# Optimization experiments

Measured on AMD Instinct MI355X. Metric: run time of the kernel, lower is better.

Reference implementation:

```python
import jax, jax.numpy as jnp
import numpy as np

B, N_PER, DEG, F_IN, F_HID = 64, 1024, 16, 128, 128
E = B * N_PER * DEG  # 1,048,576 edges, grouped per graph


def setup_inputs() -> dict:
    key = jax.random.key(0)
    ks = jax.random.split(key, 16)
    n_total = B * N_PER
    x = jax.random.normal(ks[0], (n_total, F_IN), dtype=jnp.float32)
    # edges are random within each graph block
    local = jax.random.randint(ks[1], (2, E), 0, N_PER)
    offs = (jnp.arange(E, dtype=jnp.int64) // (N_PER * DEG)) * N_PER
    edge_index = (local.astype(jnp.int64) + offs[None, :])
    edge_weight = jax.random.uniform(ks[2], (E,), dtype=jnp.float32)
    batch_index = jnp.repeat(jnp.arange(B, dtype=jnp.int64), N_PER)
    s = 1.0 / np.sqrt(F_HID)
    params = {
        'W1': jax.random.normal(ks[3], (F_IN, F_HID)) * s,
        'b1': jnp.zeros((F_HID,), jnp.float32),
        'p1': jax.random.normal(ks[4], (F_HID,)) * s,
        'W2': jax.random.normal(ks[5], (F_HID, F_HID)) * s,
        'b2': jnp.zeros((F_HID,), jnp.float32),
        'p2': jax.random.normal(ks[6], (F_HID,)) * s,
        'W3': jax.random.normal(ks[7], (F_HID, F_HID)) * s,
        'b3': jnp.zeros((F_HID,), jnp.float32),
        'p3': jax.random.normal(ks[8], (F_HID,)) * s,
        'Wo': jax.random.normal(ks[9], (2 * F_HID, 1)) * s,
        'bo': jnp.zeros((1,), jnp.float32),
    }
    return {'x': x, 'edge_index': edge_index, 'edge_weight': edge_weight,
            'batch_index': batch_index, **params}


def _gcn_conv(x, src, dst, w, W, b):
    # GCNConv with add_self_loops=True, symmetric normalization, edge_weight.
    n = x.shape[0]
    xW = x @ W
    deg = jnp.zeros((n,), x.dtype).at[dst].add(w) + 1.0  # +1 from self-loop fill
    dinv = jax.lax.rsqrt(deg)
    norm = dinv[src] * w * dinv[dst]
    agg = jnp.zeros_like(xW).at[dst].add(norm[:, None] * xW[src])
    return agg + (dinv * dinv)[:, None] * xW + b  # self-loop term + bias


def _topk_pool(x, src, dst, w, p, n, k):
    # TopKPooling with nonlinearity=sigmoid, equal-size graphs (n -> k nodes).
    f = x.shape[1]
    xr = x.reshape(B, n, f)
    score = jax.nn.sigmoid((xr @ p) / jnp.linalg.norm(p))  # [B, n]
    vals, perm = jax.lax.top_k(score, k)                    # per-graph top-k
    xn = jnp.take_along_axis(xr, perm[:, :, None], axis=1) * vals[:, :, None]
    # inverse map old local idx -> new local idx (-1 if dropped)
    inv = jnp.full((B, n), -1, dtype=jnp.int32)
    inv = inv.at[jnp.arange(B)[:, None], perm].set(jnp.arange(k, dtype=jnp.int32)[None, :])
    g = src // n
    sl = inv[g, src % n]
    dl = inv[dst // n, dst % n]
    keep = (sl >= 0) & (dl >= 0)
    # dropped edges are masked to node 0 with weight 0 (contribute nothing)
    src2 = jnp.where(keep, g * k + sl, 0)
    dst2 = jnp.where(keep, (dst // n) * k + dl, 0)
    w2 = jnp.where(keep, w, jnp.zeros((), w.dtype))
    return xn.reshape(B * k, f), src2, dst2, w2


def reference(x, edge_index, edge_weight, batch_index,
              W1, b1, p1, W2, b2, p2, W3, b3, p3, Wo, bo):
    src, dst = edge_index[0], edge_index[1]
    w = edge_weight
    n = N_PER
    h = _gcn_conv(x, src, dst, w, W1, b1)
    h, src, dst, w = _topk_pool(h, src, dst, w, p1, n, n // 2); n //= 2
    h = jax.nn.relu(h)
    h = _gcn_conv(h, src, dst, w, W2, b2)
    h, src, dst, w = _topk_pool(h, src, dst, w, p2, n, n // 2); n //= 2
    h = jax.nn.relu(h)
    h = _gcn_conv(h, src, dst, w, W3, b3)
    h, src, dst, w = _topk_pool(h, src, dst, w, p3, n, n // 2); n //= 2
    h = jax.nn.relu(h)
    hr = h.reshape(B, n, -1)
    cat = jnp.concatenate([hr.max(axis=1), hr.mean(axis=1)], axis=1)  # gmp || gap
    out = jax.nn.sigmoid(cat @ Wo + bo)
    return out, cat
```

## Files before the change

kernel.cpp:

```cpp
#include <hip/hip_runtime.h>

#define NB 64
#define EDGES 1048576
#define NTOT  65536

struct __align__(8) CsrE { int s; float w; };

using bf16x8 = __attribute__((ext_vector_type(8))) short;
using f32x4  = __attribute__((ext_vector_type(4))) float;

__global__ void k_zerof(float* __restrict__ p, int n){
  int i=blockIdx.x*256+threadIdx.x; if(i<n) p[i]=0.f;
}

__device__ inline void split1(float x, unsigned &hi16, unsigned &lo16){
  unsigned b=__float_as_uint(x);
  unsigned h=(b+0x7FFFu+((b>>16)&1u))&0xFFFF0000u;
  float lf=x-__uint_as_float(h);
  unsigned lb=__float_as_uint(lf);
  hi16=h>>16;
  lo16=(lb+0x7FFFu+((lb>>16)&1u))>>16;
}

__device__ inline void split8(const float4&u, const float4&v, bf16x8&hi, bf16x8&lo){
  float e[8]={u.x,u.y,u.z,u.w,v.x,v.y,v.z,v.w};
  #pragma unroll
  for(int j=0;j<8;++j){
    unsigned h16,l16; split1(e[j],h16,l16);
    hi[j]=(short)h16; lo[j]=(short)l16;
  }
}

template<bool G, int S>
__global__ __launch_bounds__(256) void mm_mfma(const float* __restrict__ X,
        const float* __restrict__ W, const int* __restrict__ selold,
        const float* __restrict__ score, float* __restrict__ Y, int gshift){
  __shared__ __align__(16) unsigned Wl[16384];
  const int RPB = 64*S;
  int b=blockIdx.x;
  int xcd=b&7, slot=b>>3, bpg=1<<gshift;
  int graph=xcd*8+(slot>>gshift), idx=slot&(bpg-1);
  int row0b = graph*(bpg*RPB) + idx*RPB;
  for(int t=threadIdx.x;t<8192;t+=256){
    int i=t&3, l=(t>>2)&63, c=(t>>8)&7, q=(t>>11)&3;
    int col=c*16+(l&15);
    int k0=q*32+((l>>4)<<3)+i*2;
    float x0=W[k0*128+col], x1=W[(k0+1)*128+col];
    unsigned h0,l0,h1,l1;
    split1(x0,h0,l0); split1(x1,h1,l1);
    int base=((q*8+c)*2)*256;
    Wl[base + l*4 + i]       = (h1<<16)|h0;
    Wl[base + 256 + l*4 + i] = (l1<<16)|l0;
  }
  const int wave=threadIdx.x>>6, lane=threadIdx.x&63;
  const int row0 = row0b + wave*(16*S);
  const int lrow=lane&15, lko=(lane>>4)<<3;
  int orow[S]; float scr[S];
  #pragma unroll
  for(int s=0;s<S;++s){
    int rr=row0+s*16+lrow;
    orow[s]=G?selold[rr]:rr;
    scr[s]=G?score[orow[s]]:1.f;
  }
  const f32x4 vzero={0.f,0.f,0.f,0.f};
  f32x4 acc[S][8];
  #pragma unroll
  for(int s=0;s<S;++s){
    #pragma unroll
    for(int c=0;c<8;++c) acc[s][c]=vzero;
  }
  __syncthreads();
  const char* wb=(const char*)Wl + lane*16;
  float4 u[S],v[S];
  #pragma unroll
  for(int s=0;s<S;++s){
    const float* xp=X+(size_t)orow[s]*128+lko;
    u[s]=*(const float4*)xp; v[s]=*(const float4*)(xp+4);
  }
  #pragma unroll
  for(int q=0;q<4;++q){
    float4 un[S],vn[S];
    if(q<3){
      #pragma unroll
      for(int s=0;s<S;++s){
        const float* xp=X+(size_t)orow[s]*128+(q+1)*32+lko;
        un[s]=*(const float4*)xp; vn[s]=*(const float4*)(xp+4);
      }
    }
    bf16x8 Ah[S],Al[S];
    #pragma unroll
    for(int s=0;s<S;++s){
      if(G){
        u[s].x=fmaxf(u[s].x*scr[s],0.f); u[s].y=fmaxf(u[s].y*scr[s],0.f);
        u[s].z=fmaxf(u[s].z*scr[s],0.f); u[s].w=fmaxf(u[s].w*scr[s],0.f);
        v[s].x=fmaxf(v[s].x*scr[s],0.f); v[s].y=fmaxf(v[s].y*scr[s],0.f);
        v[s].z=fmaxf(v[s].z*scr[s],0.f); v[s].w=fmaxf(v[s].w*scr[s],0.f);
      }
      split8(u[s],v[s],Ah[s],Al[s]);
    }
    #pragma unroll
    for(int c=0;c<8;++c){
      const bf16x8 bh=*(const bf16x8*)(wb + (q*8+c)*2048);
      const bf16x8 bl=*(const bf16x8*)(wb + (q*8+c)*2048 + 1024);
      #pragma unroll
      for(int s=0;s<S;++s){
        acc[s][c]=__builtin_amdgcn_mfma_f32_16x16x32_bf16(Ah[s],bh,acc[s][c],0,0,0);
        acc[s][c]=__builtin_amdgcn_mfma_f32_16x16x32_bf16(Al[s],bh,acc[s][c],0,0,0);
        acc[s][c]=__builtin_amdgcn_mfma_f32_16x16x32_bf16(Ah[s],bl,acc[s][c],0,0,0);
      }
    }
    if(q<3){
      #pragma unroll
      for(int s=0;s<S;++s){ u[s]=un[s]; v[s]=vn[s]; }
    }
  }
  const int dcol=lane&15, dr0=(lane>>4)<<2;
  #pragma unroll
  for(int s=0;s<S;++s){
    #pragma unroll
    for(int c=0;c<8;++c){
      #pragma unroll
      for(int r=0;r<4;++r){
        Y[(size_t)(row0+s*16+dr0+r)*128 + c*16 + dcol]=acc[s][c][r];
      }
    }
  }
}

__global__ __launch_bounds__(1024) void k_csr(const int* __restrict__ esrc,
        const int* __restrict__ edst, const float* __restrict__ ew,
        int* __restrict__ rowptr, float* __restrict__ dinv1, CsrE* __restrict__ csr){
  __shared__ int lc[1024];
  __shared__ float lw[1024];
  __shared__ int wsum[16];
  int g=blockIdx.x, i=threadIdx.x;
  int lane=i&63, w=i>>6;
  int e0=g*16384;
  lc[i]=0; lw[i]=0.f;
  __syncthreads();
  for(int e=e0+i; e<e0+16384; e+=1024){
    int dl=edst[e]&1023;
    atomicAdd(&lc[dl],1);
    atomicAdd(&lw[dl],ew[e]);
  }
  __syncthreads();
  int c=lc[i]; float wsv=lw[i];
  int v=c;
  #pragma unroll
  for(int off=1;off<64;off<<=1){ int t=__shfl_up(v,off,64); if(lane>=off) v+=t; }
  if(lane==63) wsum[w]=v;
  __syncthreads();
  int base=0;
  for(int k=0;k<w;++k) base+=wsum[k];
  int excl=base+v-c;
  rowptr[g*1024+i]=e0+excl;
  dinv1[g*1024+i]=rsqrtf(wsv+1.0f);
  if(g==63 && i==1023) rowptr[65536]=EDGES;
  __syncthreads();
  lc[i]=e0+excl;
  __syncthreads();
  for(int e=e0+i; e<e0+16384; e+=1024){
    int dl=edst[e]&1023;
    int pos=atomicAdd(&lc[dl],1);
    CsrE ce; ce.s=esrc[e]; ce.w=ew[e];
    csr[pos]=ce;
  }
}

template<bool F>
__global__ __launch_bounds__(256) void k_gather(const float* __restrict__ xw, const CsrE* __restrict__ csr,
        const int* __restrict__ rowptr, const int* __restrict__ map, const int* __restrict__ inv,
        const float* __restrict__ dinvv, const float* __restrict__ bias, const float* __restrict__ p,
        float* __restrict__ h, float* __restrict__ score, int gshift, int ns){
  int wv=threadIdx.x>>6, half=(threadIdx.x>>5)&1, hl=threadIdx.x&31;
  int b=blockIdx.x, xcd=b&7, slot=b>>3, bpg=1<<gshift;
  int graph=xcd*8+(slot>>gshift), idx=slot&(bpg-1);
  int v = graph*(bpg<<3) + (idx<<3) + wv*2 + half;
  if(v>=ns) return;
  int d0 = F? map[v] : v;
  float dv=dinvv[v];
  int rs=rowptr[d0], re=rowptr[d0+1];
  const int f4=hl*4;
  float4 accA={0.f,0.f,0.f,0.f}, accB={0.f,0.f,0.f,0.f};
  for(int base=rs; base<re; base+=32){
    int len=re-base; if(len>32) len=32;
    int sidx=0; float cf=0.f;
    if(hl<len){
      CsrE en=csr[base+hl];
      int s=en.s; bool live=true;
      if(F){ int t=inv[s]; live=(t>=0); s=live?t:0; }
      if(live){ sidx=s; cf=dinvv[s]*en.w; }
    }
    int len8=(len+7)&~7;
    for(int j=0;j<len8;j+=8){
      float cc[8]; int ss[8];
      #pragma unroll
      for(int m=0;m<8;++m){ cc[m]=__shfl(cf,j+m,32); ss[m]=__shfl(sidx,j+m,32); }
      float4 xv_[8];
      #pragma unroll
      for(int m=0;m<8;++m) xv_[m]=*(const float4*)&xw[(size_t)ss[m]*128+f4];
      #pragma unroll
      for(int m=0;m<8;m+=2){
        accA.x+=cc[m]*xv_[m].x; accA.y+=cc[m]*xv_[m].y;
        accA.z+=cc[m]*xv_[m].z; accA.w+=cc[m]*xv_[m].w;
        accB.x+=cc[m+1]*xv_[m+1].x; accB.y+=cc[m+1]*xv_[m+1].y;
        accB.z+=cc[m+1]*xv_[m+1].z; accB.w+=cc[m+1]*xv_[m+1].w;
      }
    }
  }
  float4 acc; acc.x=accA.x+accB.x; acc.y=accA.y+accB.y;
  acc.z=accA.z+accB.z; acc.w=accA.w+accB.w;
  const float4 xv=*(const float4*)&xw[(size_t)v*128+f4];
  const float4 bv=*(const float4*)&bias[f4];
  float d2=dv*dv;
  float4 hv;
  hv.x=acc.x*dv + d2*xv.x + bv.x;
  hv.y=acc.y*dv + d2*xv.y + bv.y;
  hv.z=acc.z*dv + d2*xv.z + bv.z;
  hv.w=acc.w*dv + d2*xv.w + bv.w;
  *(float4*)&h[(size_t)v*128+f4]=hv;
  const float4 pv=*(const float4*)&p[f4];
  float z=hv.x*pv.x+hv.y*pv.y+hv.z*pv.z+hv.w*pv.w;
  float pp=pv.x*pv.x+pv.y*pv.y+pv.z*pv.z+pv.w*pv.w;
  #pragma unroll
  for(int m=16;m>0;m>>=1){ z+=__shfl_xor(z,m,32); pp+=__shfl_xor(pp,m,32); }
  if(hl==0) score[v]=1.0f/(1.0f+expf(-z/sqrtf(pp)));
}

template<int N, int K, int MODE>
__global__ __launch_bounds__(N) void k_topk(const float* __restrict__ score,
        int* __restrict__ inv, int* __restrict__ selold,
        const int* __restrict__ inv1s, const int* __restrict__ sel1s,
        int* __restrict__ inv12, int* __restrict__ map12,
        const int* __restrict__ rowptr, const CsrE* __restrict__ csr,
        float* __restrict__ dinv_out,
        const float* __restrict__ h3, const float* __restrict__ Wo,
        const float* __restrict__ bo, float* __restrict__ outp){
  __shared__ unsigned hist[256];
  __shared__ int wsum[16];
  __shared__ int c_sh, r_sh;
  __shared__ float red2[256];
  __shared__ int sOld[128];
  __shared__ float sSc[128];
  int g=blockIdx.x, i=threadIdx.x;
  int lane=i&63, w=i>>6;
  int gv=g*N+i;
  unsigned key=__float_as_uint(score[gv]);
  int st=1;
  int R=K;
  #pragma unroll
  for(int pass=0; pass<4; ++pass){
    int shift=24-pass*8;
    if(i<256) hist[i]=0;
    __syncthreads();
    unsigned byte=(key>>shift)&255u;
    if(st==1) atomicAdd(&hist[byte],1u);
    __syncthreads();
    unsigned hcnt=0, sfx=0;
    if(i<256){
      hcnt=hist[i]; sfx=hcnt;
      #pragma unroll
      for(int off=1;off<64;off<<=1){
        unsigned t=__shfl_down(sfx,off,64);
        if(lane+off<64) sfx+=t;
      }
      if(lane==0) wsum[w]=(int)sfx;
    }
    __syncthreads();
    if(i<256){
      int tot=0;
      for(int k=w+1;k<4;++k) tot+=wsum[k];
      int Si=(int)sfx+tot;
      int A=Si-(int)hcnt;
      if(A<R && R<=Si){ c_sh=i; r_sh=R-A; }
    }
    __syncthreads();
    int c=c_sh; R=r_sh;
    if(st==1){
      if((int)byte>c) st=2;
      else if((int)byte<c) st=0;
    }
    __syncthreads();
  }
  int alive=(st==1)?1:0;
  unsigned long long mA=__ballot(alive);
  int rA=__popcll(mA & ((1ULL<<lane)-1ULL));
  if(lane==0) wsum[w]=__popcll(mA);
  __syncthreads();
  int offA=0;
  for(int k=0;k<w;++k) offA+=wsum[k];
  int tie_rank=offA+rA;
  int sel=(st==2)||(st==1 && tie_rank<R);
  __syncthreads();
  unsigned long long mS=__ballot(sel);
  int rS=__popcll(mS & ((1ULL<<lane)-1ULL));
  if(lane==0) wsum[w]=__popcll(mS);
  __syncthreads();
  int offS=0;
  for(int k=0;k<w;++k) offS+=wsum[k];
  int ng=g*K+offS+rS;
  if(sel && ng<NB*K){ inv[gv]=ng; selold[ng]=gv; }
  else inv[gv]=-1;
  if(MODE==1){
    __syncthreads();
    for(int t=i; t<K; t+=N){
      int v=g*K+t;
      int d0=selold[v];
      int rs=rowptr[d0], re=rowptr[d0+1];
      float s0=0.f,s1=0.f,s2=0.f,s3=0.f;
      int e=rs;
      for(; e+4<=re; e+=4){
        CsrE e0=csr[e], e1=csr[e+1], e2=csr[e+2], e3=csr[e+3];
        if(inv[e0.s]>=0) s0+=e0.w;
        if(inv[e1.s]>=0) s1+=e1.w;
        if(inv[e2.s]>=0) s2+=e2.w;
        if(inv[e3.s]>=0) s3+=e3.w;
      }
      for(; e<re; ++e){
        CsrE en=csr[e];
        if(inv[en.s]>=0) s0+=en.w;
      }
      dinv_out[v]=rsqrtf((s0+s1)+(s2+s3)+1.0f);
    }
  }
  if(MODE==2){
    __syncthreads();
    for(int t=i; t<1024; t+=N){
      int v0=g*1024+t;
      int q=inv1s[v0];
      inv12[v0]=(q>=0)?inv[q]:-1;
    }
    for(int t=i; t<K; t+=N){
      int v=g*K+t;
      map12[v]=sel1s[selold[v]];
    }
    __syncthreads();
    for(int t=i; t<K; t+=N){
      int v=g*K+t;
      int d0=map12[v];
      int rs=rowptr[d0], re=rowptr[d0+1];
      float s0=0.f,s1=0.f,s2=0.f,s3=0.f;
      int e=rs;
      for(; e+4<=re; e+=4){
        CsrE e0=csr[e], e1=csr[e+1], e2=csr[e+2], e3=csr[e+3];
        if(inv12[e0.s]>=0) s0+=e0.w;
        if(inv12[e1.s]>=0) s1+=e1.w;
        if(inv12[e2.s]>=0) s2+=e2.w;
        if(inv12[e3.s]>=0) s3+=e3.w;
      }
      for(; e<re; ++e){
        CsrE en=csr[e];
        if(inv12[en.s]>=0) s0+=en.w;
      }
      dinv_out[v]=rsqrtf((s0+s1)+(s2+s3)+1.0f);
    }
  }
  if(MODE==3){
    __syncthreads();
    if(i<128){ int o=selold[g*128+i]; sOld[i]=o; sSc[i]=score[o]; }
    __syncthreads();
    int f=i&127, hf=i>>7;
    float mx=-3.4e38f, sm=0.f;
    #pragma unroll 4
    for(int nd=hf*64; nd<hf*64+64; ++nd){
      float vv=fmaxf(h3[(size_t)sOld[nd]*128+f]*sSc[nd],0.f);
      mx=fmaxf(mx,vv); sm+=vv;
    }
    red2[i]=mx; __syncthreads();
    float mx2 = (hf==0)? fmaxf(mx,red2[i+128]) : 0.f;
    __syncthreads();
    red2[i]=sm; __syncthreads();
    if(hf==0){
      float smT=sm+red2[i+128];
      float mean=smT*(1.0f/128.0f);
      outp[64+g*256+f]    =mx2;
      outp[64+g*256+128+f]=mean;
    }
    __syncthreads();
    if(hf==0) red2[f]=mx2*Wo[f]+( (sm+red2[f+128]) * (1.0f/128.0f))*Wo[128+f];
    __syncthreads();
    for(int off=64;off>0;off>>=1){
      if(i<off) red2[i]+=red2[i+off];
      __syncthreads();
    }
    if(i==0){ float z=red2[0]+bo[0]; outp[g]=1.0f/(1.0f+expf(-z)); }
  }
}

extern "C" void kernel_launch(void* const* d_in, const int* in_sizes, int n_in,
                              void* d_out, int out_size, void* d_ws, size_t ws_size,
                              hipStream_t stream) {
  (void)in_sizes; (void)n_in;
  const float* x  = (const float*)d_in[0];
  const int*   ei = (const int*)d_in[1];
  const float* ew = (const float*)d_in[2];
  const float* W1=(const float*)d_in[4];  const float* b1=(const float*)d_in[5];  const float* p1=(const float*)d_in[6];
  const float* W2=(const float*)d_in[7];  const float* b2=(const float*)d_in[8];  const float* p2=(const float*)d_in[9];
  const float* W3=(const float*)d_in[10]; const float* b3=(const float*)d_in[11]; const float* p3=(const float*)d_in[12];
  const float* Wo=(const float*)d_in[13]; const float* bo=(const float*)d_in[14];
  float* out=(float*)d_out;

  char* ws=(char*)d_ws;
  size_t cur=0;
  float* slot0=(float*)(ws+cur); cur+=33554432;
  float* slot1=(float*)(ws+cur); cur+=33554432;
  CsrE*  csr  =(CsrE*)(ws+cur);  cur+=(size_t)EDGES*8;
  int*   rowptr=(int*) (ws+cur); cur+=262400;
  float* dinv1=(float*)(ws+cur); cur+=262144;
  float* dinv2=(float*)(ws+cur); cur+=131072;
  float* dinv3=(float*)(ws+cur); cur+=65536;
  float* sc1  =(float*)(ws+cur); cur+=262144;
  float* sc2  =(float*)(ws+cur); cur+=131072;
  float* sc3  =(float*)(ws+cur); cur+=65536;
  int*   inv1 =(int*)  (ws+cur); cur+=262144;
  int*   inv2 =(int*)  (ws+cur); cur+=131072;
  int*   invS =(int*)  (ws+cur); cur+=65536;
  int*   inv12=(int*)  (ws+cur); cur+=262144;
  int*   sel1 =(int*)  (ws+cur); cur+=131072;
  int*   sel2 =(int*)  (ws+cur); cur+=65536;
  int*   sel3 =(int*)  (ws+cur); cur+=32768;
  int*   map12=(int*)  (ws+cur); cur+=65536;

  if (ws_size < cur) {
    k_zerof<<<(out_size+255)/256,256,0,stream>>>(out,out_size);
    return;
  }

  const int* esrc=ei; const int* edst=ei+EDGES;

  mm_mfma<false,2><<<NTOT/128,256,0,stream>>>(x,W1,nullptr,nullptr,slot0,3);
  k_csr<<<NB,1024,0,stream>>>(esrc,edst,ew,rowptr,dinv1,csr);
  k_gather<false><<<NTOT/8,256,0,stream>>>(slot0,csr,rowptr,nullptr,nullptr,
                                           dinv1,b1,p1,slot1,sc1,7,NTOT);
  k_topk<1024,512,1><<<NB,1024,0,stream>>>(sc1,inv1,sel1,nullptr,nullptr,nullptr,nullptr,
                                           rowptr,csr,dinv2,nullptr,nullptr,nullptr,nullptr);

  mm_mfma<true,1><<<32768/64,256,0,stream>>>(slot1,W2,sel1,sc1,slot0,3);
  k_gather<true><<<32768/8,256,0,stream>>>(slot0,csr,rowptr,sel1,inv1,
                                           dinv2,b2,p2,slot1,sc2,6,32768);
  k_topk<512,256,2><<<NB,512,0,stream>>>(sc2,inv2,sel2,inv1,sel1,inv12,map12,
                                         rowptr,csr,dinv3,nullptr,nullptr,nullptr,nullptr);

  mm_mfma<true,1><<<16384/64,256,0,stream>>>(slot1,W3,sel2,sc2,slot0,2);
  k_gather<true><<<16384/8,256,0,stream>>>(slot0,csr,rowptr,map12,inv12,
                                           dinv3,b3,p3,slot1,sc3,5,16384);
  k_topk<256,128,3><<<NB,256,0,stream>>>(sc3,invS,sel3,nullptr,nullptr,nullptr,nullptr,
                                         nullptr,nullptr,nullptr,slot1,Wo,bo,out);
}
```

Baseline: 311.6 us.

## Split CSR build into chunked count, scan, and global-atomic scatter kernels

The single 64-block CSR construction kernel becomes three kernels: a 256-block per-chunk degree count, a per-graph scan that sums the four chunk counts, and a 256-block scatter that uses global atomics on fill pointers. The goal is to spread the edge-processing work over four times as many blocks, since 64 blocks leave most of the GPU's compute units idle. In exchange it adds two kernel launches, extra global traffic for the chunk arrays, and slower global atomics in place of LDS atomics during the scatter.

Result: no change. 309.5 us (-0.7%).

```diff
diff --git a/kernel.cpp b/kernel.cpp
--- a/kernel.cpp
+++ b/kernel.cpp
@@ -127,24 +127,35 @@
   }
 }
 
-__global__ __launch_bounds__(1024) void k_csr(const int* __restrict__ esrc,
-        const int* __restrict__ edst, const float* __restrict__ ew,
-        int* __restrict__ rowptr, float* __restrict__ dinv1, CsrE* __restrict__ csr){
+__global__ __launch_bounds__(1024) void k_count(const int* __restrict__ edst,
+        const float* __restrict__ ew, int* __restrict__ chunkcnt, float* __restrict__ chunkw){
   __shared__ int lc[1024];
   __shared__ float lw[1024];
+  int b=blockIdx.x, i=threadIdx.x;
+  int xcd=b&7, slot=b>>3;
+  int graph=xcd*8+(slot&7), chunk=slot>>3;
+  int e0=graph*16384+chunk*4096;
+  lc[i]=0; lw[i]=0.f;
+  __syncthreads();
+  for(int e=e0+i; e<e0+4096; e+=1024){
+    int dl=edst[e]&1023;
+    atomicAdd(&lc[dl],1);
+    atomicAdd(&lw[dl],ew[e]);
+  }
+  __syncthreads();
+  chunkcnt[chunk*65536+graph*1024+i]=lc[i];
+  chunkw  [chunk*65536+graph*1024+i]=lw[i];
+}
+
+__global__ __launch_bounds__(1024) void k_scan_graph(const int* __restrict__ chunkcnt,
+        const float* __restrict__ chunkw, int* __restrict__ rowptr,
+        float* __restrict__ dinv1, int* __restrict__ fill){
   __shared__ int wsum[16];
   int g=blockIdx.x, i=threadIdx.x;
   int lane=i&63, w=i>>6;
-  int e0=g*16384;
-  lc[i]=0; lw[i]=0.f;
-  __syncthreads();
-  for(int e=e0+i; e<e0+16384; e+=1024){
-    int dl=edst[e]&1023;
-    atomicAdd(&lc[dl],1);
-    atomicAdd(&lw[dl],ew[e]);
-  }
-  __syncthreads();
-  int c=lc[i]; float wsv=lw[i];
+  int o=g*1024+i;
+  int c = chunkcnt[o]+chunkcnt[65536+o]+chunkcnt[131072+o]+chunkcnt[196608+o];
+  float ws = chunkw[o]+chunkw[65536+o]+chunkw[131072+o]+chunkw[196608+o];
   int v=c;
   #pragma unroll
   for(int off=1;off<64;off<<=1){ int t=__shfl_up(v,off,64); if(lane>=off) v+=t; }
@@ -153,15 +164,24 @@
   int base=0;
   for(int k=0;k<w;++k) base+=wsum[k];
   int excl=base+v-c;
-  rowptr[g*1024+i]=e0+excl;
-  dinv1[g*1024+i]=rsqrtf(wsv+1.0f);
+  int e0=g*16384;
+  rowptr[o]=e0+excl;
+  fill[o]=e0+excl;
+  dinv1[o]=rsqrtf(ws+1.0f);
   if(g==63 && i==1023) rowptr[65536]=EDGES;
-  __syncthreads();
-  lc[i]=e0+excl;
-  __syncthreads();
-  for(int e=e0+i; e<e0+16384; e+=1024){
+}
+
+__global__ __launch_bounds__(1024) void k_scatter2(const int* __restrict__ esrc,
+        const int* __restrict__ edst, const float* __restrict__ ew,
+        int* __restrict__ fill, CsrE* __restrict__ csr){
+  int b=blockIdx.x, i=threadIdx.x;
+  int xcd=b&7, slot=b>>3;
+  int graph=xcd*8+(slot&7), chunk=slot>>3;
+  int e0=graph*16384+chunk*4096;
+  int base=graph*1024;
+  for(int e=e0+i; e<e0+4096; e+=1024){
     int dl=edst[e]&1023;
-    int pos=atomicAdd(&lc[dl],1);
+    int pos=atomicAdd(&fill[base+dl],1);
     CsrE ce; ce.s=esrc[e]; ce.w=ew[e];
     csr[pos]=ce;
   }
@@ -405,6 +425,9 @@
   float* slot0=(float*)(ws+cur); cur+=33554432;
   float* slot1=(float*)(ws+cur); cur+=33554432;
   CsrE*  csr  =(CsrE*)(ws+cur);  cur+=(size_t)EDGES*8;
+  int*   chunkcnt=(int*)(ws+cur); cur+=1048576;
+  float* chunkw  =(float*)(ws+cur); cur+=1048576;
+  int*   fill =(int*)  (ws+cur); cur+=262144;
   int*   rowptr=(int*) (ws+cur); cur+=262400;
   float* dinv1=(float*)(ws+cur); cur+=262144;
   float* dinv2=(float*)(ws+cur); cur+=131072;
@@ -429,7 +452,9 @@
   const int* esrc=ei; const int* edst=ei+EDGES;
 
   mm_mfma<false,2><<<NTOT/128,256,0,stream>>>(x,W1,nullptr,nullptr,slot0,3);
-  k_csr<<<NB,1024,0,stream>>>(esrc,edst,ew,rowptr,dinv1,csr);
+  k_count<<<256,1024,0,stream>>>(edst,ew,chunkcnt,chunkw);
+  k_scan_graph<<<64,1024,0,stream>>>(chunkcnt,chunkw,rowptr,dinv1,fill);
+  k_scatter2<<<256,1024,0,stream>>>(esrc,edst,ew,fill,csr);
   k_gather<false><<<NTOT/8,256,0,stream>>>(slot0,csr,rowptr,nullptr,nullptr,
                                            dinv1,b1,p1,slot1,sc1,7,NTOT);
   k_topk<1024,512,1><<<NB,1024,0,stream>>>(sc1,inv1,sel1,nullptr,nullptr,nullptr,nullptr,
```

## Split CSR build into chunked count/scatter kernels, prepack weights, fuse with first matmul

Applied to the files above, without the earlier changes.

The single 64-block CSR construction kernel is replaced by two passes: a 512-block per-chunk histogram (degree counts and weight sums), then a scatter pass that computes prefix offsets from the chunk counts and fills the CSR. The scatter pass shares a launch with the first matmul, so the two run concurrently across more CUs. The bf16 hi/lo weight split is now done once for all three layers in the histogram kernel, and every matmul just copies the prepacked tile into LDS. In exchange it writes about 4 MB of extra chunk-count scratch and adds a launch, and edge order within a CSR row changes, which can shift float summation order.

Result: faster. 271.8 us (-12.8%).

```diff
diff --git a/kernel.cpp b/kernel.cpp
--- a/kernel.cpp
+++ b/kernel.cpp
@@ -31,27 +31,191 @@
   }
 }
 
+__global__ __launch_bounds__(256) void k_cntpack(const int* __restrict__ edst,
+        const float* __restrict__ ew, int* __restrict__ chunkcnt, float* __restrict__ chunkw,
+        const float* __restrict__ W1, const float* __restrict__ W2,
+        const float* __restrict__ W3, unsigned* __restrict__ outp){
+  __shared__ int lc[1024];
+  __shared__ float lw[1024];
+  int b=blockIdx.x, tid=threadIdx.x;
+  if(b<512){
+    int xcd=b&7, slot=b>>3;
+    int graph=xcd*8+(slot&7), chunk=slot>>3;
+    int e0=graph*16384+chunk*2048;
+    for(int t=tid;t<1024;t+=256){ lc[t]=0; lw[t]=0.f; }
+    __syncthreads();
+    for(int e=e0+tid; e<e0+2048; e+=256){
+      int dl=edst[e]&1023;
+      atomicAdd(&lc[dl],1);
+      atomicAdd(&lw[dl],ew[e]);
+    }
+    __syncthreads();
+    for(int t=tid;t<1024;t+=256){
+      chunkcnt[chunk*65536+graph*1024+t]=lc[t];
+      chunkw  [chunk*65536+graph*1024+t]=lw[t];
+    }
+  } else {
+    int wb=b-512, m=wb>>3;
+    const float* W = (m==0)?W1:((m==1)?W2:W3);
+    unsigned* o = outp + m*16384;
+    for(int t=(wb&7)*256+tid; t<8192; t+=2048){
+      int i=t&3, l=(t>>2)&63, c=(t>>8)&7, q=(t>>11)&3;
+      int col=c*16+(l&15);
+      int k0=q*32+((l>>4)<<3)+i*2;
+      float x0=W[k0*128+col], x1=W[(k0+1)*128+col];
+      unsigned h0,l0,h1,l1;
+      split1(x0,h0,l0); split1(x1,h1,l1);
+      int base=((q*8+c)*2)*256;
+      o[base + l*4 + i]       = (h1<<16)|h0;
+      o[base + 256 + l*4 + i] = (l1<<16)|l0;
+    }
+  }
+}
+
+__global__ __launch_bounds__(256) void k_mm1scat(const float* __restrict__ X,
+        const unsigned* __restrict__ Wpk,
+        const int* __restrict__ esrc, const int* __restrict__ edst,
+        const float* __restrict__ ew, const int* __restrict__ chunkcnt,
+        const float* __restrict__ chunkw, int* __restrict__ rowptr,
+        float* __restrict__ dinv1, CsrE* __restrict__ csr,
+        float* __restrict__ Y){
+  __shared__ __align__(16) unsigned Wl[16384];
+  int b=blockIdx.x;
+  if(b<512){
+    const int RPB=128;
+    int row0b=b*RPB;
+    for(int t=threadIdx.x;t<4096;t+=256)
+      ((uint4*)Wl)[t]=((const uint4*)Wpk)[t];
+    const int wave=threadIdx.x>>6, lane=threadIdx.x&63;
+    const int row0=row0b+wave*32;
+    const int lrow=lane&15, lko=(lane>>4)<<3;
+    int orow[2];
+    #pragma unroll
+    for(int s=0;s<2;++s) orow[s]=row0+s*16+lrow;
+    const f32x4 vzero={0.f,0.f,0.f,0.f};
+    f32x4 acc[2][8];
+    #pragma unroll
+    for(int s=0;s<2;++s){
+      #pragma unroll
+      for(int c=0;c<8;++c) acc[s][c]=vzero;
+    }
+    __syncthreads();
+    const char* wb=(const char*)Wl + lane*16;
+    float4 u[2],v[2];
+    #pragma unroll
+    for(int s=0;s<2;++s){
+      const float* xp=X+(size_t)orow[s]*128+lko;
+      u[s]=*(const float4*)xp; v[s]=*(const float4*)(xp+4);
+    }
+    #pragma unroll
+    for(int q=0;q<4;++q){
+      float4 un[2],vn[2];
+      if(q<3){
+        #pragma unroll
+        for(int s=0;s<2;++s){
+          const float* xp=X+(size_t)orow[s]*128+(q+1)*32+lko;
+          un[s]=*(const float4*)xp; vn[s]=*(const float4*)(xp+4);
+        }
+      }
+      bf16x8 Ah[2],Al[2];
+      #pragma unroll
+      for(int s=0;s<2;++s) split8(u[s],v[s],Ah[s],Al[s]);
+      #pragma unroll
+      for(int c=0;c<8;++c){
+        const bf16x8 bh=*(const bf16x8*)(wb + (q*8+c)*2048);
+        const bf16x8 bl=*(const bf16x8*)(wb + (q*8+c)*2048 + 1024);
+        #pragma unroll
+        for(int s=0;s<2;++s){
+          acc[s][c]=__builtin_amdgcn_mfma_f32_16x16x32_bf16(Ah[s],bh,acc[s][c],0,0,0);
+          acc[s][c]=__builtin_amdgcn_mfma_f32_16x16x32_bf16(Al[s],bh,acc[s][c],0,0,0);
+          acc[s][c]=__builtin_amdgcn_mfma_f32_16x16x32_bf16(Ah[s],bl,acc[s][c],0,0,0);
+        }
+      }
+      if(q<3){
+        #pragma unroll
+        for(int s=0;s<2;++s){ u[s]=un[s]; v[s]=vn[s]; }
+      }
+    }
+    const int dcol=lane&15, dr0=(lane>>4)<<2;
+    #pragma unroll
+    for(int s=0;s<2;++s){
+      #pragma unroll
+      for(int c=0;c<8;++c){
+        #pragma unroll
+        for(int r=0;r<4;++r){
+          Y[(size_t)(row0+s*16+dr0+r)*128 + c*16 + dcol]=acc[s][c][r];
+        }
+      }
+    }
+  } else {
+    int* lc=(int*)Wl;
+    int* wsum=(int*)Wl+1024;
+    int sb=b-512, i=threadIdx.x;
+    int lane=i&63, w=i>>6;
+    int xcd=sb&7, slot=sb>>3;
+    int graph=xcd*8+(slot&7), chunk=slot>>3;
+    int n0=4*i, o0=graph*1024+n0;
+    int ck[4][8], csum[4];
+    int tot=0;
+    #pragma unroll
+    for(int j=0;j<4;++j){
+      int c=0;
+      #pragma unroll
+      for(int k=0;k<8;++k){ int t=chunkcnt[k*65536+o0+j]; ck[j][k]=t; c+=t; }
+      csum[j]=c; tot+=c;
+    }
+    int v=tot;
+    #pragma unroll
+    for(int off=1;off<64;off<<=1){ int t=__shfl_up(v,off,64); if(lane>=off) v+=t; }
+    if(lane==63) wsum[w]=v;
+    __syncthreads();
+    int base=0;
+    for(int k=0;k<w;++k) base+=wsum[k];
+    int texcl=base+v-tot;
+    int run=texcl;
+    #pragma unroll
+    for(int j=0;j<4;++j){
+      int r0=graph*16384+run;
+      if(chunk==0){
+        rowptr[o0+j]=r0;
+        float wsv=0.f;
+        #pragma unroll
+        for(int k=0;k<8;++k) wsv+=chunkw[k*65536+o0+j];
+        dinv1[o0+j]=rsqrtf(wsv+1.0f);
+      }
+      int myfill=r0;
+      #pragma unroll
+      for(int k=0;k<8;++k) if(k<chunk) myfill+=ck[j][k];
+      lc[n0+j]=myfill;
+      run+=csum[j];
+    }
+    if(graph==63 && chunk==0 && i==255) rowptr[65536]=EDGES;
+    __syncthreads();
+    int e0=graph*16384+chunk*2048;
+    for(int e=e0+i; e<e0+2048; e+=256){
+      int dl=edst[e]&1023;
+      int pos=atomicAdd(&lc[dl],1);
+      CsrE ce; ce.s=esrc[e]; ce.w=ew[e];
+      csr[pos]=ce;
+    }
+  }
+}
+
 template<bool G, int S>
 __global__ __launch_bounds__(256) void mm_mfma(const float* __restrict__ X,
-        const float* __restrict__ W, const int* __restrict__ selold,
+        const unsigned* __restrict__ Wpk, const int* __restrict__ selold,
         const float* __restrict__ score, float* __restrict__ Y, int gshift){
   __shared__ __align__(16) unsigned Wl[16384];
   const int RPB = 64*S;
   int b=blockIdx.x;
-  int xcd=b&7, slot=b>>3, bpg=1<<gshift;
-  int graph=xcd*8+(slot>>gshift), idx=slot&(bpg-1);
-  int row0b = graph*(bpg*RPB) + idx*RPB;
-  for(int t=threadIdx.x;t<8192;t+=256){
-    int i=t&3, l=(t>>2)&63, c=(t>>8)&7, q=(t>>11)&3;
-    int col=c*16+(l&15);
-    int k0=q*32+((l>>4)<<3)+i*2;
-    float x0=W[k0*128+col], x1=W[(k0+1)*128+col];
-    unsigned h0,l0,h1,l1;
-    split1(x0,h0,l0); split1(x1,h1,l1);
-    int base=((q*8+c)*2)*256;
-    Wl[base + l*4 + i]       = (h1<<16)|h0;
-    Wl[base + 256 + l*4 + i] = (l1<<16)|l0;
-  }
+  int row0b;
+  if(G){
+    int xcd=b&7, slot=b>>3, bpg=1<<gshift;
+    int graph=xcd*8+(slot>>gshift), idx=slot&(bpg-1);
+    row0b = graph*(bpg*RPB) + idx*RPB;
+  } else row0b = b*RPB;
+  for(int t=threadIdx.x;t<4096;t+=256)
+    ((uint4*)Wl)[t]=((const uint4*)Wpk)[t];
   const int wave=threadIdx.x>>6, lane=threadIdx.x&63;
   const int row0 = row0b + wave*(16*S);
   const int lrow=lane&15, lko=(lane>>4)<<3;
@@ -124,46 +288,6 @@
         Y[(size_t)(row0+s*16+dr0+r)*128 + c*16 + dcol]=acc[s][c][r];
       }
     }
-  }
-}
-
-__global__ __launch_bounds__(1024) void k_csr(const int* __restrict__ esrc,
-        const int* __restrict__ edst, const float* __restrict__ ew,
-        int* __restrict__ rowptr, float* __restrict__ dinv1, CsrE* __restrict__ csr){
-  __shared__ int lc[1024];
-  __shared__ float lw[1024];
-  __shared__ int wsum[16];
-  int g=blockIdx.x, i=threadIdx.x;
-  int lane=i&63, w=i>>6;
-  int e0=g*16384;
-  lc[i]=0; lw[i]=0.f;
-  __syncthreads();
-  for(int e=e0+i; e<e0+16384; e+=1024){
-    int dl=edst[e]&1023;
-    atomicAdd(&lc[dl],1);
-    atomicAdd(&lw[dl],ew[e]);
-  }
-  __syncthreads();
-  int c=lc[i]; float wsv=lw[i];
-  int v=c;
-  #pragma unroll
-  for(int off=1;off<64;off<<=1){ int t=__shfl_up(v,off,64); if(lane>=off) v+=t; }
-  if(lane==63) wsum[w]=v;
-  __syncthreads();
-  int base=0;
-  for(int k=0;k<w;++k) base+=wsum[k];
-  int excl=base+v-c;
-  rowptr[g*1024+i]=e0+excl;
-  dinv1[g*1024+i]=rsqrtf(wsv+1.0f);
-  if(g==63 && i==1023) rowptr[65536]=EDGES;
-  __syncthreads();
-  lc[i]=e0+excl;
-  __syncthreads();
-  for(int e=e0+i; e<e0+16384; e+=1024){
-    int dl=edst[e]&1023;
-    int pos=atomicAdd(&lc[dl],1);
-    CsrE ce; ce.s=esrc[e]; ce.w=ew[e];
-    csr[pos]=ce;
   }
 }
 
@@ -405,6 +529,8 @@
   float* slot0=(float*)(ws+cur); cur+=33554432;
   float* slot1=(float*)(ws+cur); cur+=33554432;
   CsrE*  csr  =(CsrE*)(ws+cur);  cur+=(size_t)EDGES*8;
+  int*   chunkcnt=(int*)(ws+cur); cur+=2097152;
+  float* chunkw  =(float*)(ws+cur); cur+=2097152;
   int*   rowptr=(int*) (ws+cur); cur+=262400;
   float* dinv1=(float*)(ws+cur); cur+=262144;
   float* dinv2=(float*)(ws+cur); cur+=131072;
@@ -420,6 +546,7 @@
   int*   sel2 =(int*)  (ws+cur); cur+=65536;
   int*   sel3 =(int*)  (ws+cur); cur+=32768;
   int*   map12=(int*)  (ws+cur); cur+=65536;
+  unsigned* wpk=(unsigned*)(ws+cur); cur+=196608;
 
   if (ws_size < cur) {
     k_zerof<<<(out_size+255)/256,256,0,stream>>>(out,out_size);
@@ -428,20 +555,21 @@
 
   const int* esrc=ei; const int* edst=ei+EDGES;
 
-  mm_mfma<false,2><<<NTOT/128,256,0,stream>>>(x,W1,nullptr,nullptr,slot0,3);
-  k_csr<<<NB,1024,0,stream>>>(esrc,edst,ew,rowptr,dinv1,csr);
+  k_cntpack<<<536,256,0,stream>>>(edst,ew,chunkcnt,chunkw,W1,W2,W3,wpk);
+  k_mm1scat<<<1024,256,0,stream>>>(x,wpk,esrc,edst,ew,chunkcnt,chunkw,
+                                   rowptr,dinv1,csr,slot0);
   k_gather<false><<<NTOT/8,256,0,stream>>>(slot0,csr,rowptr,nullptr,nullptr,
                                            dinv1,b1,p1,slot1,sc1,7,NTOT);
   k_topk<1024,512,1><<<NB,1024,0,stream>>>(sc1,inv1,sel1,nullptr,nullptr,nullptr,nullptr,
                                            rowptr,csr,dinv2,nullptr,nullptr,nullptr,nullptr);
 
-  mm_mfma<true,1><<<32768/64,256,0,stream>>>(slot1,W2,sel1,sc1,slot0,3);
+  mm_mfma<true,1><<<32768/64,256,0,stream>>>(slot1,wpk+16384,sel1,sc1,slot0,3);
   k_gather<true><<<32768/8,256,0,stream>>>(slot0,csr,rowptr,sel1,inv1,
                                            dinv2,b2,p2,slot1,sc2,6,32768);
   k_topk<512,256,2><<<NB,512,0,stream>>>(sc2,inv2,sel2,inv1,sel1,inv12,map12,
                                          rowptr,csr,dinv3,nullptr,nullptr,nullptr,nullptr);
 
-  mm_mfma<true,1><<<16384/64,256,0,stream>>>(slot1,W3,sel2,sc2,slot0,2);
+  mm_mfma<true,1><<<16384/64,256,0,stream>>>(slot1,wpk+32768,sel2,sc2,slot0,2);
   k_gather<true><<<16384/8,256,0,stream>>>(slot0,csr,rowptr,map12,inv12,
                                            dinv3,b3,p3,slot1,sc3,5,16384);
   k_topk<256,128,3><<<NB,256,0,stream>>>(sc3,invS,sel3,nullptr,nullptr,nullptr,nullptr,
```
